# Optimization experiments

Measured on AMD Instinct MI355X. Metric: run time of the kernel, lower is better.

Reference implementation:

```python
import jax, jax.numpy as jnp
import numpy as np

IMAGE_SIZE = 224
COV_HP = 1.0
SIGMA = 1.0
STEPS = 2
CUTOFF = 20.0
IMP_LO, IMP_HI = 0.5, 2.0
REL_W = 0.5
EPS = 1e-6

# Projection matrices for front/top/left views (buffer Js in the module)
JS = jnp.array([[[1, 0, 0], [0, 1, 0]],
                [[1, 0, 0], [0, 0, 1]],
                [[0, 0, 1], [0, 1, 0]]], dtype=jnp.float32)


def _blur(d, sigma):
    # d: [B,H,W]; separable Gaussian blur, 'same' padding
    r = max(1, int(3 * sigma))
    x = jnp.arange(-r, r + 1, dtype=jnp.float32)
    k = jnp.exp(-(x * x) / (2.0 * sigma * sigma))
    k = k / k.sum()
    d4 = d[:, None]  # [B,1,H,W]
    kh = k.reshape(1, 1, -1, 1)
    kw = k.reshape(1, 1, 1, -1)
    d4 = jax.lax.conv_general_dilated(d4, kh, (1, 1), [(r, r), (0, 0)],
                                      dimension_numbers=('NCHW', 'OIHW', 'NCHW'))
    d4 = jax.lax.conv_general_dilated(d4, kw, (1, 1), [(0, 0), (r, r)],
                                      dimension_numbers=('NCHW', 'OIHW', 'NCHW'))
    return d4[:, 0]


def _fill_depth_map(d, sigma, steps):
    # fill_depth_map is not defined in the source; implemented as iterative
    # Gaussian-blur hole filling (empty pixels take blurred neighborhood).
    for _ in range(steps):
        b = _blur(d, sigma)
        d = jnp.where(d > 1e-6, d, b)
    return d


def _forward(position, cov3d, opacity, importance):
    B, N, _ = position.shape
    H = W = IMAGE_SIZE
    Hh, Wh = H // 2, W // 2
    yy, xx = jnp.meshgrid(jnp.arange(Hh), jnp.arange(Wh), indexing='ij')
    grid = jnp.stack([xx, yy], axis=-1).astype(jnp.float32)  # [Hh,Wh,2]
    imp = jnp.clip(jnp.broadcast_to(importance[:, :N], (B, N)), IMP_LO, IMP_HI)
    imp = imp[:, :, None, None]
    eye3 = jnp.eye(3, dtype=cov3d.dtype)
    eye2 = jnp.eye(2, dtype=cov3d.dtype)
    maps = []
    for v in range(3):  # fixed small view loop, as in the source
        J = JS[v]  # [2,3]
        # NOTE: source mutates cov3d across the view loop; replicate that
        cov3d = (cov3d + jnp.swapaxes(cov3d, -1, -2)) * 0.5
        cov3d = cov3d + EPS * eye3
        nrm = jnp.linalg.norm(cov3d, axis=(-1, -2), keepdims=True)
        cov3d = cov3d / (nrm + EPS) * COV_HP
        cinv = jnp.linalg.inv(cov3d)                               # [B,N,3,3]
        cov2d_inv = jnp.einsum('ij,bnjk,lk->bnil', J, cinv, J)     # J C^-1 J^T
        cov2d_inv = cov2d_inv + eye2 * (EPS * 1e-4)
        proj = jnp.einsum('bnk,jk->bnj', position, J)              # [B,N,2]
        mn = proj.min(axis=1, keepdims=True)
        mx = proj.max(axis=1, keepdims=True)
        rng = mx - mn + 1e-6
        mn = mn - 0.5 * rng
        mx = mx + 0.5 * rng
        rng = mx - mn + 1e-6
        xy = jnp.clip((proj - mn) / rng * (Wh - 1), 0.0, Wh - 1)
        delta = grid[None, None] - xy[:, :, None, None, :]         # [B,N,Hh,Wh,2]
        mask_h = jnp.linalg.norm(delta, axis=-1) < CUTOFF
        mask = jnp.repeat(jnp.repeat(mask_h, 2, axis=2), 2, axis=3)
        exph = -jnp.einsum('bnhwj,bnjk,bnhwk->bnhw', delta, cov2d_inv, delta)
        exp_full = jax.image.resize(exph, (B, N, H, W), method='bilinear')
        exp_full = jnp.clip(exp_full, -20.0, 0.0)
        w = opacity[:, :, None, None] * imp * jnp.exp(exp_full)
        w = jnp.where(mask, w, 0.0)
        wmin = w.min(axis=1, keepdims=True)
        wmax = w.max(axis=1, keepdims=True)
        nw = (w - wmin) / (wmax - wmin + EPS) * REL_W + w / (w.sum(axis=1, keepdims=True) + EPS)
        dm = nw.sum(axis=1)  # [B,H,W]
        maps.append(_fill_depth_map(dm, SIGMA, STEPS))
    d = jnp.stack(maps, axis=1)  # [B,3,H,W], already 224x224 so resize is a no-op
    d = (d - d.mean()) / (jnp.std(d, ddof=1) + EPS)
    return d


def setup_inputs() -> dict:
    key = jax.random.key(0)
    k1, k2, k3 = jax.random.split(key, 3)
    B, N, MAXG = 1, 512, 1000
    return {
        'position': jax.random.normal(k1, (B, N, 3), dtype=jnp.float32),
        'cov3d': jax.random.normal(k2, (B, N, 3, 3), dtype=jnp.float32),
        'opacity': jax.random.uniform(k3, (B, N), dtype=jnp.float32),
        'importance': jnp.ones((1, MAXG), dtype=jnp.float32),
    }


def reference(position, cov3d, opacity, importance):
    return _forward(position, cov3d, opacity, importance)
```

## Files before the change

### kernel.cpp

```cpp
#include <hip/hip_runtime.h>
#include <math.h>


__device__ __forceinline__ float wave_min(float v) {
    #pragma unroll
    for (int o = 32; o >= 1; o >>= 1) v = fminf(v, __shfl_xor(v, o));
    return v;
}

__global__ __launch_bounds__(512) void splat_fused_kernel(
    const float* __restrict__ position, const float* __restrict__ cov3d,
    const float* __restrict__ opacity, const float* __restrict__ importance,
    float* __restrict__ dm) {
    __shared__ float ls[512 * 8];
    __shared__ float red[8 * 6];
    __shared__ float pS[3][128], pMn[3][128], pMx[3][128];
    __shared__ int cnt;
    const int v = blockIdx.z;
    const int tx0 = blockIdx.x * 16, ty0 = blockIdx.y * 8;
    const int tid = threadIdx.x;
    const int lane = tid & 63, wave = tid >> 6;

    const int n = tid;
    const float p0 = position[n * 3 + 0];
    const float p1 = position[n * 3 + 1];
    const float p2 = position[n * 3 + 2];
    const float opimp = opacity[n] * fminf(fmaxf(importance[n], 0.5f), 2.0f);

    {
        float vals[6] = {p0, -p0, p1, -p1, p2, -p2};
        #pragma unroll
        for (int k = 0; k < 6; ++k) {
            float r = wave_min(vals[k]);
            if (lane == 0) red[wave * 6 + k] = r;
        }
    }
    __syncthreads();
    float mn6[6];
    #pragma unroll
    for (int k = 0; k < 6; ++k) {
        float r = red[k];
        #pragma unroll
        for (int w = 1; w < 8; ++w) r = fminf(r, red[w * 6 + k]);
        mn6[k] = r;
    }
    const float pmn[3] = {mn6[0], mn6[2], mn6[4]};
    const float pmx[3] = {-mn6[1], -mn6[3], -mn6[5]};

    float c00 = cov3d[n * 9 + 0], c01 = cov3d[n * 9 + 1], c02 = cov3d[n * 9 + 2];
    float c10 = cov3d[n * 9 + 3], c11 = cov3d[n * 9 + 4], c12 = cov3d[n * 9 + 5];
    float c20 = cov3d[n * 9 + 6], c21 = cov3d[n * 9 + 7], c22 = cov3d[n * 9 + 8];
    for (int vv = 0; vv <= v; ++vv) {
        float s01 = 0.5f * (c01 + c10);
        float s02 = 0.5f * (c02 + c20);
        float s12 = 0.5f * (c12 + c21);
        float s00 = c00 + 1e-6f;
        float s11 = c11 + 1e-6f;
        float s22 = c22 + 1e-6f;
        float nrm = sqrtf(s00 * s00 + s11 * s11 + s22 * s22 +
                          2.0f * (s01 * s01 + s02 * s02 + s12 * s12));
        float inv = 1.0f / (nrm + 1e-6f);
        c00 = s00 * inv; c11 = s11 * inv; c22 = s22 * inv;
        c01 = s01 * inv; c10 = c01; c02 = s02 * inv; c20 = c02;
        c12 = s12 * inv; c21 = c12;
    }
    float cof00 = c11 * c22 - c12 * c12;
    float cof01 = c02 * c12 - c01 * c22;
    float cof02 = c01 * c12 - c02 * c11;
    float det = c00 * cof00 + c01 * cof01 + c02 * cof02;
    float idet = 1.0f / det;
    float i00 = cof00 * idet;
    float i01 = cof01 * idet;
    float i02 = cof02 * idet;
    float i11 = (c00 * c22 - c02 * c02) * idet;
    float i12 = (c02 * c01 - c00 * c12) * idet;
    float i22 = (c00 * c11 - c01 * c01) * idet;

    float Aa, Ab, Ac, prx, pry;
    int ix, iy;
    if (v == 0)      { Aa = i00; Ab = i01; Ac = i11; prx = p0; pry = p1; ix = 0; iy = 1; }
    else if (v == 1) { Aa = i00; Ab = i02; Ac = i22; prx = p0; pry = p2; ix = 0; iy = 2; }
    else             { Aa = i22; Ab = i12; Ac = i11; prx = p2; pry = p1; ix = 2; iy = 1; }
    Aa += 1e-10f;
    Ac += 1e-10f;

    float mnx = pmn[ix], mxx = pmx[ix], mny = pmn[iy], mxy = pmx[iy];
    float rngx = mxx - mnx + 1e-6f;
    float mnx2 = mnx - 0.5f * rngx;
    float mxx2 = mxx + 0.5f * rngx;
    rngx = mxx2 - mnx2 + 1e-6f;
    float rngy = mxy - mny + 1e-6f;
    float mny2 = mny - 0.5f * rngy;
    float mxy2 = mxy + 0.5f * rngy;
    rngy = mxy2 - mny2 + 1e-6f;
    float gx = fminf(fmaxf((prx - mnx2) / rngx * 111.0f, 0.0f), 111.0f);
    float gy = fminf(fmaxf((pry - mny2) / rngy * 111.0f, 0.0f), 111.0f);

    if (tid == 0) cnt = 0;
    __syncthreads();
    {
        const float bx0 = (float)(tx0 >> 1), bx1 = (float)((tx0 + 15) >> 1);
        const float by0 = (float)(ty0 >> 1), by1 = (float)((ty0 + 7) >> 1);
        float dx = fmaxf(fmaxf(bx0 - gx, gx - bx1), 0.0f);
        float dy = fmaxf(fmaxf(by0 - gy, gy - by1), 0.0f);
        bool pass = (dx * dx + dy * dy) < 400.01f;
        unsigned long long m = __ballot(pass);
        int base = 0;
        if (lane == 0) base = atomicAdd(&cnt, __popcll(m));
        base = __shfl(base, 0);
        if (pass) {
            int slot = base + __popcll(m & ((1ull << lane) - 1ull));
            float4* d = (float4*)&ls[slot * 8];
            d[0] = make_float4(Aa, 2.0f * Ab, Ac, gx);
            d[1] = make_float4(gy, opimp, 0.0f, 0.0f);
        }
    }
    __syncthreads();
    const int len = cnt;
    const int npad = (len + 15) & ~15;
    if (tid < npad - len) {
        float4* d = (float4*)&ls[(len + tid) * 8];
        d[0] = make_float4(1.0f, 0.0f, 1.0f, 1e9f);
        d[1] = make_float4(1e9f, 0.0f, 0.0f, 0.0f);
    }
    __syncthreads();

    const int r = wave >> 1;
    const int pid = (wave & 1) * 64 + lane;
    const int xo = tx0 + (pid & 15);
    const int yo = ty0 + (pid >> 4);
    const int xh = xo >> 1, yh = yo >> 1;
    const int px = xo & 1, py = yo & 1;
    int xlo = xh - 1 + px; int xhi = min(xlo + 1, 111); xlo = max(xlo, 0);
    int ylo = yh - 1 + py; int yhi = min(ylo + 1, 111); ylo = max(ylo, 0);
    const float wxlo = px ? 0.75f : 0.25f, wxhi = 1.0f - wxlo;
    const float wylo = py ? 0.75f : 0.25f, wyhi = 1.0f - wylo;
    const float fx0 = (float)xlo, fx1 = (float)xhi;
    const float fy0 = (float)ylo, fy1 = (float)yhi;
    const float ex = wxlo * fx0 + wxhi * fx1;
    const float ey = wylo * fy0 + wyhi * fy1;
    const float Vx = wxlo * wxhi * (fx1 - fx0) * (fx1 - fx0);
    const float Vy = wylo * wyhi * (fy1 - fy0) * (fy1 - fy0);
    const float fxh = (float)xh, fyh = (float)yh;

    float S = 0.0f, wmn = INFINITY, wmx = -INFINITY;
    const float4* lsv = (const float4*)ls;
    for (int base = r * 4; base < npad; base += 16) {
        float4 ga[4], gb[4];
        #pragma unroll
        for (int k = 0; k < 4; ++k) {
            ga[k] = lsv[2 * (base + k)];
            gb[k] = lsv[2 * (base + k) + 1];
        }
        #pragma unroll
        for (int k = 0; k < 4; ++k) {
            const float xx = ga[k].w, yy = gb[k].x;
            const float dxh = fxh - xx, dyh = fyh - yy;
            float w = 0.0f;
            if (dxh * dxh + dyh * dyh < 400.0f) {
                const float dx = ex - xx, dy = ey - yy;
                float q = dx * (ga[k].x * dx + ga[k].y * dy) + ga[k].z * dy * dy;
                float bil = -(q + ga[k].x * Vx + ga[k].z * Vy);
                bil = fminf(fmaxf(bil, -20.0f), 0.0f);
                w = gb[k].y * __expf(bil);
            }
            S += w; wmn = fminf(wmn, w); wmx = fmaxf(wmx, w);
        }
    }
    if (r > 0) { pS[r - 1][pid] = S; pMn[r - 1][pid] = wmn; pMx[r - 1][pid] = wmx; }
    __syncthreads();
    if (r == 0) {
        #pragma unroll
        for (int k = 0; k < 3; ++k) {
            S += pS[k][pid];
            wmn = fminf(wmn, pMn[k][pid]);
            wmx = fmaxf(wmx, pMx[k][pid]);
        }
        if (len < 512) { wmn = fminf(wmn, 0.0f); wmx = fmaxf(wmx, 0.0f); }
        float dmv = 0.5f * (S - 512.0f * wmn) / (wmx - wmn + 1e-6f) + S / (S + 1e-6f);
        dm[(v * 224 + yo) * 224 + xo] = dmv;
    }
}

__global__ __launch_bounds__(256) void blur2_stats_kernel(
    const float* __restrict__ in, float* __restrict__ out,
    float2* __restrict__ partials) {
    __shared__ float A[44 * 45];
    __shared__ float T[44 * 45];
    __shared__ float r1[4], r2[4];
    const int v = blockIdx.z;
    const int tx0 = blockIdx.x * 32, ty0 = blockIdx.y * 32;
    const int tid = threadIdx.x;
    const float kw[7] = {0.00443305f, 0.05400558f, 0.24203623f, 0.39905030f,
                         0.24203623f, 0.05400558f, 0.00443305f};
    const float* __restrict__ chan = in + v * 224 * 224;

    for (int idx = tid; idx < 44 * 44; idx += 256) {
        int rr = idx / 44, c = idx % 44;
        int gyy = ty0 - 6 + rr, gxx = tx0 - 6 + c;
        float val = 0.0f;
        if (gyy >= 0 && gyy < 224 && gxx >= 0 && gxx < 224) val = chan[gyy * 224 + gxx];
        A[rr * 45 + c] = val;
    }
    __syncthreads();
    for (int idx = tid; idx < 38 * 44; idx += 256) {
        int rr = 3 + idx / 44, c = idx % 44;
        float s = 0.0f;
        #pragma unroll
        for (int i = 0; i < 7; ++i) s += kw[i] * A[(rr - 3 + i) * 45 + c];
        T[rr * 45 + c] = s;
    }
    __syncthreads();
    for (int idx = tid; idx < 38 * 38; idx += 256) {
        int rr = 3 + idx / 38, c = 3 + idx % 38;
        float s = 0.0f;
        #pragma unroll
        for (int j = 0; j < 7; ++j) s += kw[j] * T[rr * 45 + c - 3 + j];
        float ctr = A[rr * 45 + c];
        A[rr * 45 + c] = ctr > 1e-6f ? ctr : s;
    }
    __syncthreads();
    for (int idx = tid; idx < 32 * 38; idx += 256) {
        int rr = 6 + idx / 38, c = 3 + idx % 38;
        float s = 0.0f;
        #pragma unroll
        for (int i = 0; i < 7; ++i) s += kw[i] * A[(rr - 3 + i) * 45 + c];
        T[rr * 45 + c] = s;
    }
    __syncthreads();
    float ls1 = 0.0f, ls2 = 0.0f;
    for (int idx = tid; idx < 32 * 32; idx += 256) {
        int rr = 6 + (idx >> 5), c = 6 + (idx & 31);
        float s = 0.0f;
        #pragma unroll
        for (int j = 0; j < 7; ++j) s += kw[j] * T[rr * 45 + c - 3 + j];
        float ctr = A[rr * 45 + c];
        float d2 = ctr > 1e-6f ? ctr : s;
        out[(v * 224 + ty0 + rr - 6) * 224 + (tx0 + c - 6)] = d2;
        ls1 += d2; ls2 += d2 * d2;
    }
    #pragma unroll
    for (int o = 32; o >= 1; o >>= 1) {
        ls1 += __shfl_xor(ls1, o);
        ls2 += __shfl_xor(ls2, o);
    }
    if ((tid & 63) == 0) { r1[tid >> 6] = ls1; r2[tid >> 6] = ls2; }
    __syncthreads();
    if (tid == 0) {
        float s1 = r1[0] + r1[1] + r1[2] + r1[3];
        float s2 = r2[0] + r2[1] + r2[2] + r2[3];
        partials[(blockIdx.z * 7 + blockIdx.y) * 7 + blockIdx.x] = make_float2(s1, s2);
    }
}

__global__ __launch_bounds__(256) void normalize_kernel(
    const float2* __restrict__ partials, float* __restrict__ out) {
    __shared__ double s1[256], s2[256];
    const int tid = threadIdx.x;
    double a = 0.0, b = 0.0;
    if (tid < 147) {
        float2 p = partials[tid];
        a = (double)p.x; b = (double)p.y;
    }
    s1[tid] = a; s2[tid] = b;
    __syncthreads();
    for (int s = 128; s >= 1; s >>= 1) {
        if (tid < s) { s1[tid] += s1[tid + s]; s2[tid] += s2[tid + s]; }
        __syncthreads();
    }
    const double M = 150528.0;
    double mean = s1[0] / M;
    double var = (s2[0] - M * mean * mean) / (M - 1.0);
    double sd = sqrt(var > 0.0 ? var : 0.0);
    const int idx = blockIdx.x * 256 + tid;
    if (idx < 3 * 224 * 224)
        out[idx] = (out[idx] - (float)mean) / ((float)sd + 1e-6f);
}

extern "C" void kernel_launch(void* const* d_in, const int* in_sizes, int n_in,
                              void* d_out, int out_size, void* d_ws, size_t ws_size,
                              hipStream_t stream) {
    const float* position   = (const float*)d_in[0];
    const float* cov3d      = (const float*)d_in[1];
    const float* opacity    = (const float*)d_in[2];
    const float* importance = (const float*)d_in[3];
    float* out = (float*)d_out;

    float* dmA       = (float*)d_ws;
    float2* partials = (float2*)((float*)d_ws + 150528);

    hipLaunchKernelGGL(splat_fused_kernel, dim3(14, 28, 3), dim3(512), 0, stream,
                       position, cov3d, opacity, importance, dmA);
    hipLaunchKernelGGL(blur2_stats_kernel, dim3(7, 7, 3), dim3(256), 0, stream,
                       dmA, out, partials);
    hipLaunchKernelGGL(normalize_kernel, dim3(588), dim3(256), 0, stream,
                       partials, out);
}
```

Baseline: 99.62 us.

## Shrink splat and blur tiles, split gaussians across 8 waves, branchless weights

The splat kernel now handles an 8x8 pixel tile per block, with all 8 waves splitting the gaussian list (8-way instead of 4-way) and reducing partials across waves. Gaussian data is repacked into separate float4/float2 shared arrays, and the per-gaussian cutoff branch becomes a select. Empty tiles exit early. The blur kernel moves to 16x16 tiles with more blocks and explicit zeroing of out-of-image halo after the first fill pass. The normalize kernel loops over the larger partials array. Together this raises block count and parallelism, at the cost of more redundant per-block setup (recomputing all 512 gaussians per block, twice as many blocks) and a larger halo-to-tile ratio in the blur.

```diff
diff --git a/kernel.cpp b/kernel.cpp
--- a/kernel.cpp
+++ b/kernel.cpp
@@ -12,12 +12,13 @@
     const float* __restrict__ position, const float* __restrict__ cov3d,
     const float* __restrict__ opacity, const float* __restrict__ importance,
     float* __restrict__ dm) {
-    __shared__ float ls[512 * 8];
+    __shared__ float4 lsA[512];
+    __shared__ float2 lsB[512];
     __shared__ float red[8 * 6];
-    __shared__ float pS[3][128], pMn[3][128], pMx[3][128];
+    __shared__ float pS[7][64], pMn[7][64], pMx[7][64];
     __shared__ int cnt;
     const int v = blockIdx.z;
-    const int tx0 = blockIdx.x * 16, ty0 = blockIdx.y * 8;
+    const int tx0 = blockIdx.x * 8, ty0 = blockIdx.y * 8;
     const int tid = threadIdx.x;
     const int lane = tid & 63, wave = tid >> 6;
 
@@ -99,7 +100,7 @@
     if (tid == 0) cnt = 0;
     __syncthreads();
     {
-        const float bx0 = (float)(tx0 >> 1), bx1 = (float)((tx0 + 15) >> 1);
+        const float bx0 = (float)(tx0 >> 1), bx1 = (float)((tx0 + 7) >> 1);
         const float by0 = (float)(ty0 >> 1), by1 = (float)((ty0 + 7) >> 1);
         float dx = fmaxf(fmaxf(bx0 - gx, gx - bx1), 0.0f);
         float dy = fmaxf(fmaxf(by0 - gy, gy - by1), 0.0f);
@@ -110,25 +111,29 @@
         base = __shfl(base, 0);
         if (pass) {
             int slot = base + __popcll(m & ((1ull << lane) - 1ull));
-            float4* d = (float4*)&ls[slot * 8];
-            d[0] = make_float4(Aa, 2.0f * Ab, Ac, gx);
-            d[1] = make_float4(gy, opimp, 0.0f, 0.0f);
+            lsA[slot] = make_float4(Aa, 2.0f * Ab, Ac, opimp);
+            lsB[slot] = make_float2(gx, gy);
         }
     }
     __syncthreads();
     const int len = cnt;
-    const int npad = (len + 15) & ~15;
+
+    const int rep = wave;
+    const int xo = tx0 + (lane & 7);
+    const int yo = ty0 + (lane >> 3);
+
+    if (len == 0) {
+        if (rep == 0) dm[(v * 224 + yo) * 224 + xo] = 0.0f;
+        return;
+    }
+
+    const int npad = (len + 31) & ~31;
     if (tid < npad - len) {
-        float4* d = (float4*)&ls[(len + tid) * 8];
-        d[0] = make_float4(1.0f, 0.0f, 1.0f, 1e9f);
-        d[1] = make_float4(1e9f, 0.0f, 0.0f, 0.0f);
-    }
-    __syncthreads();
-
-    const int r = wave >> 1;
-    const int pid = (wave & 1) * 64 + lane;
-    const int xo = tx0 + (pid & 15);
-    const int yo = ty0 + (pid >> 4);
+        lsA[len + tid] = make_float4(1.0f, 0.0f, 1.0f, 0.0f);
+        lsB[len + tid] = make_float2(1e9f, 1e9f);
+    }
+    __syncthreads();
+
     const int xh = xo >> 1, yh = yo >> 1;
     const int px = xo & 1, py = yo & 1;
     int xlo = xh - 1 + px; int xhi = min(xlo + 1, 111); xlo = max(xlo, 0);
@@ -144,37 +149,36 @@
     const float fxh = (float)xh, fyh = (float)yh;
 
     float S = 0.0f, wmn = INFINITY, wmx = -INFINITY;
-    const float4* lsv = (const float4*)ls;
-    for (int base = r * 4; base < npad; base += 16) {
-        float4 ga[4], gb[4];
+    for (int base = rep * 4; base < npad; base += 32) {
+        float4 ga[4];
+        float2 gb[4];
         #pragma unroll
         for (int k = 0; k < 4; ++k) {
-            ga[k] = lsv[2 * (base + k)];
-            gb[k] = lsv[2 * (base + k) + 1];
+            ga[k] = lsA[base + k];
+            gb[k] = lsB[base + k];
         }
         #pragma unroll
         for (int k = 0; k < 4; ++k) {
-            const float xx = ga[k].w, yy = gb[k].x;
+            const float xx = gb[k].x, yy = gb[k].y;
             const float dxh = fxh - xx, dyh = fyh - yy;
-            float w = 0.0f;
-            if (dxh * dxh + dyh * dyh < 400.0f) {
-                const float dx = ex - xx, dy = ey - yy;
-                float q = dx * (ga[k].x * dx + ga[k].y * dy) + ga[k].z * dy * dy;
-                float bil = -(q + ga[k].x * Vx + ga[k].z * Vy);
-                bil = fminf(fmaxf(bil, -20.0f), 0.0f);
-                w = gb[k].y * __expf(bil);
-            }
+            const bool m = dxh * dxh + dyh * dyh < 400.0f;
+            const float dx = ex - xx, dy = ey - yy;
+            float q = dx * (ga[k].x * dx + ga[k].y * dy) + ga[k].z * dy * dy;
+            float bil = -(q + ga[k].x * Vx + ga[k].z * Vy);
+            bil = fminf(fmaxf(bil, -20.0f), 0.0f);
+            bil = m ? bil : -1e9f;
+            float w = ga[k].w * __expf(bil);
             S += w; wmn = fminf(wmn, w); wmx = fmaxf(wmx, w);
         }
     }
-    if (r > 0) { pS[r - 1][pid] = S; pMn[r - 1][pid] = wmn; pMx[r - 1][pid] = wmx; }
-    __syncthreads();
-    if (r == 0) {
-        #pragma unroll
-        for (int k = 0; k < 3; ++k) {
-            S += pS[k][pid];
-            wmn = fminf(wmn, pMn[k][pid]);
-            wmx = fmaxf(wmx, pMx[k][pid]);
+    if (rep > 0) { pS[rep - 1][lane] = S; pMn[rep - 1][lane] = wmn; pMx[rep - 1][lane] = wmx; }
+    __syncthreads();
+    if (rep == 0) {
+        #pragma unroll
+        for (int k = 0; k < 7; ++k) {
+            S += pS[k][lane];
+            wmn = fminf(wmn, pMn[k][lane]);
+            wmx = fmaxf(wmx, pMx[k][lane]);
         }
         if (len < 512) { wmn = fminf(wmn, 0.0f); wmx = fmaxf(wmx, 0.0f); }
         float dmv = 0.5f * (S - 512.0f * wmn) / (wmx - wmn + 1e-6f) + S / (S + 1e-6f);
@@ -185,56 +189,59 @@
 __global__ __launch_bounds__(256) void blur2_stats_kernel(
     const float* __restrict__ in, float* __restrict__ out,
     float2* __restrict__ partials) {
-    __shared__ float A[44 * 45];
-    __shared__ float T[44 * 45];
+    __shared__ float A[28 * 29];
+    __shared__ float T[28 * 29];
     __shared__ float r1[4], r2[4];
     const int v = blockIdx.z;
-    const int tx0 = blockIdx.x * 32, ty0 = blockIdx.y * 32;
+    const int tx0 = blockIdx.x * 16, ty0 = blockIdx.y * 16;
     const int tid = threadIdx.x;
     const float kw[7] = {0.00443305f, 0.05400558f, 0.24203623f, 0.39905030f,
                          0.24203623f, 0.05400558f, 0.00443305f};
     const float* __restrict__ chan = in + v * 224 * 224;
 
-    for (int idx = tid; idx < 44 * 44; idx += 256) {
-        int rr = idx / 44, c = idx % 44;
+    for (int idx = tid; idx < 28 * 28; idx += 256) {
+        int rr = idx / 28, c = idx % 28;
         int gyy = ty0 - 6 + rr, gxx = tx0 - 6 + c;
         float val = 0.0f;
         if (gyy >= 0 && gyy < 224 && gxx >= 0 && gxx < 224) val = chan[gyy * 224 + gxx];
-        A[rr * 45 + c] = val;
-    }
-    __syncthreads();
-    for (int idx = tid; idx < 38 * 44; idx += 256) {
-        int rr = 3 + idx / 44, c = idx % 44;
+        A[rr * 29 + c] = val;
+    }
+    __syncthreads();
+    for (int idx = tid; idx < 22 * 28; idx += 256) {
+        int rr = 3 + idx / 28, c = idx % 28;
         float s = 0.0f;
         #pragma unroll
-        for (int i = 0; i < 7; ++i) s += kw[i] * A[(rr - 3 + i) * 45 + c];
-        T[rr * 45 + c] = s;
-    }
-    __syncthreads();
-    for (int idx = tid; idx < 38 * 38; idx += 256) {
-        int rr = 3 + idx / 38, c = 3 + idx % 38;
+        for (int i = 0; i < 7; ++i) s += kw[i] * A[(rr - 3 + i) * 29 + c];
+        T[rr * 29 + c] = s;
+    }
+    __syncthreads();
+    for (int idx = tid; idx < 22 * 22; idx += 256) {
+        int rr = 3 + idx / 22, c = 3 + idx % 22;
+        int gyy = ty0 - 6 + rr, gxx = tx0 - 6 + c;
         float s = 0.0f;
         #pragma unroll
-        for (int j = 0; j < 7; ++j) s += kw[j] * T[rr * 45 + c - 3 + j];
-        float ctr = A[rr * 45 + c];
-        A[rr * 45 + c] = ctr > 1e-6f ? ctr : s;
-    }
-    __syncthreads();
-    for (int idx = tid; idx < 32 * 38; idx += 256) {
-        int rr = 6 + idx / 38, c = 3 + idx % 38;
+        for (int j = 0; j < 7; ++j) s += kw[j] * T[rr * 29 + c - 3 + j];
+        float ctr = A[rr * 29 + c];
+        float d1 = ctr > 1e-6f ? ctr : s;
+        if (gyy < 0 || gyy > 223 || gxx < 0 || gxx > 223) d1 = 0.0f;
+        A[rr * 29 + c] = d1;
+    }
+    __syncthreads();
+    for (int idx = tid; idx < 16 * 22; idx += 256) {
+        int rr = 6 + idx / 22, c = 3 + idx % 22;
         float s = 0.0f;
         #pragma unroll
-        for (int i = 0; i < 7; ++i) s += kw[i] * A[(rr - 3 + i) * 45 + c];
-        T[rr * 45 + c] = s;
+        for (int i = 0; i < 7; ++i) s += kw[i] * A[(rr - 3 + i) * 29 + c];
+        T[rr * 29 + c] = s;
     }
     __syncthreads();
     float ls1 = 0.0f, ls2 = 0.0f;
-    for (int idx = tid; idx < 32 * 32; idx += 256) {
-        int rr = 6 + (idx >> 5), c = 6 + (idx & 31);
+    for (int idx = tid; idx < 16 * 16; idx += 256) {
+        int rr = 6 + (idx >> 4), c = 6 + (idx & 15);
         float s = 0.0f;
         #pragma unroll
-        for (int j = 0; j < 7; ++j) s += kw[j] * T[rr * 45 + c - 3 + j];
-        float ctr = A[rr * 45 + c];
+        for (int j = 0; j < 7; ++j) s += kw[j] * T[rr * 29 + c - 3 + j];
+        float ctr = A[rr * 29 + c];
         float d2 = ctr > 1e-6f ? ctr : s;
         out[(v * 224 + ty0 + rr - 6) * 224 + (tx0 + c - 6)] = d2;
         ls1 += d2; ls2 += d2 * d2;
@@ -249,7 +256,7 @@
     if (tid == 0) {
         float s1 = r1[0] + r1[1] + r1[2] + r1[3];
         float s2 = r2[0] + r2[1] + r2[2] + r2[3];
-        partials[(blockIdx.z * 7 + blockIdx.y) * 7 + blockIdx.x] = make_float2(s1, s2);
+        partials[(blockIdx.z * 14 + blockIdx.y) * 14 + blockIdx.x] = make_float2(s1, s2);
     }
 }
 
@@ -258,9 +265,9 @@
     __shared__ double s1[256], s2[256];
     const int tid = threadIdx.x;
     double a = 0.0, b = 0.0;
-    if (tid < 147) {
-        float2 p = partials[tid];
-        a = (double)p.x; b = (double)p.y;
+    for (int i = tid; i < 588; i += 256) {
+        float2 p = partials[i];
+        a += (double)p.x; b += (double)p.y;
     }
     s1[tid] = a; s2[tid] = b;
     __syncthreads();
@@ -289,9 +296,9 @@
     float* dmA       = (float*)d_ws;
     float2* partials = (float2*)((float*)d_ws + 150528);
 
-    hipLaunchKernelGGL(splat_fused_kernel, dim3(14, 28, 3), dim3(512), 0, stream,
+    hipLaunchKernelGGL(splat_fused_kernel, dim3(28, 28, 3), dim3(512), 0, stream,
                        position, cov3d, opacity, importance, dmA);
-    hipLaunchKernelGGL(blur2_stats_kernel, dim3(7, 7, 3), dim3(256), 0, stream,
+    hipLaunchKernelGGL(blur2_stats_kernel, dim3(14, 14, 3), dim3(256), 0, stream,
                        dmA, out, partials);
     hipLaunchKernelGGL(normalize_kernel, dim3(588), dim3(256), 0, stream,
                        partials, out);
```

New measurement: 95.07 us. 4.6% less time.
